# Performance work log

Measured on AMD Instinct MI355X. Metric: run time of the kernel, lower is better.

Reference implementation:

```python
import jax, jax.numpy as jnp
import numpy as np

NEG = -1e30

def setup_inputs() -> dict:
    key = jax.random.key(0)
    k = jax.random.split(key, 6)
    B, Lc, Lq, D = 16, 2048, 256, 256
    c = jax.random.normal(k[0], (B, Lc, D), dtype=jnp.float32)
    q = jax.random.normal(k[1], (B, Lq, D), dtype=jnp.float32)
    c_mask = jnp.ones((B, Lc), dtype=jnp.float32)
    q_mask = jnp.ones((B, Lq), dtype=jnp.float32)
    # xavier-uniform-ish scale for the similarity weights
    lim = float(np.sqrt(6.0 / (D + 1)))
    cq_weight = jax.random.uniform(k[2], (1, 1, D), jnp.float32, -lim, lim)
    c_weight = jax.random.uniform(k[3], (1, D), jnp.float32, -lim, lim)
    q_weight = jax.random.uniform(k[4], (1, D), jnp.float32, -lim, lim)
    bias = jnp.zeros((1,), dtype=jnp.float32)
    return {"c": c, "q": q, "c_mask": c_mask, "q_mask": q_mask,
            "cq_weight": cq_weight, "c_weight": c_weight,
            "q_weight": q_weight, "bias": bias}

def _masked_softmax(logits, mask):
    # mask: 1=keep, 0=pad; broadcast over logits' leading dims
    x = logits * mask + (1.0 - mask) * NEG
    return jax.nn.softmax(x, axis=-1)

def reference(c, q, c_mask, q_mask, cq_weight, c_weight, q_weight, bias):
    # trilinear similarity S[b,i,j] = w_c.c_i + w_q.q_j + (c_i*w_cq).q_j + b
    s0 = jnp.einsum('bid,od->bio', c, c_weight)              # [B,Lc,1]
    s1 = jnp.einsum('bjd,od->boj', q, q_weight)              # [B,1,Lq]
    s2 = jnp.einsum('bid,bjd->bij', c * cq_weight, q)        # [B,Lc,Lq]
    S = s0 + s1 + s2 + bias                                  # [B,Lc,Lq]
    S1 = _masked_softmax(S, q_mask[:, None, :])              # softmax over q
    C2Q = jnp.einsum('bij,bjd->bid', S1, q)                  # [B,Lc,D]
    S2t = _masked_softmax(jnp.swapaxes(S, 1, 2), c_mask[:, None, :])  # [B,Lq,Lc]
    S2 = jnp.einsum('bij,bjk->bik', S1, S2t)                 # [B,Lc,Lc]
    Q2C = jnp.einsum('bik,bkd->bid', S2, c)                  # [B,Lc,D]
    return jnp.concatenate((c, C2Q, c * C2Q, c * Q2C), axis=-1)
```

## Files before the change

### kernel.cpp

```cpp
#include <hip/hip_runtime.h>
#include <hip/hip_bf16.h>

#define NB 16
#define LC 2048
#define LQ 256
#define DD 256
#define NEGINF -1e30f

typedef __attribute__((ext_vector_type(8))) short bf16x8;
typedef __attribute__((ext_vector_type(4))) float f32x4;

#define MFMA16(a, b, c) __builtin_amdgcn_mfma_f32_16x16x32_bf16((a), (b), (c), 0, 0, 0)

typedef const unsigned int __attribute__((address_space(1))) glb_u32;
typedef unsigned int __attribute__((address_space(3))) lds_u32;

__device__ __forceinline__ void gload_lds16(const void* g, void* l) {
    __builtin_amdgcn_global_load_lds((glb_u32*)g, (lds_u32*)l, 16, 0, 0);
}

__device__ __forceinline__ short f2b(float x) {
    unsigned u = __float_as_uint(x);
    unsigned r = (u + 0x7fffu + ((u >> 16) & 1u)) >> 16;
    return (short)r;
}
__device__ __forceinline__ float b2f(short s) {
    return __uint_as_float(((unsigned)(unsigned short)s) << 16);
}

#define NCB (NB * LC / 8)
__global__ __launch_bounds__(256) void prep(
        const float* __restrict__ c, const float* __restrict__ q,
        const float* __restrict__ c_w, const float* __restrict__ cqw,
        const float* __restrict__ q_w, const float* __restrict__ bias,
        short* __restrict__ c16, float* __restrict__ s0c,
        short* __restrict__ qw16, short* __restrict__ qT16,
        float* __restrict__ s1q, float* __restrict__ out) {
    __shared__ float T[64][65];
    int t = threadIdx.x;
    if (blockIdx.x < NCB) {
        int row = blockIdx.x * 8 + (t >> 5);
        int k = t & 31;
        const float* src = c + (size_t)row * DD + k * 8;
        float4 v0 = *(const float4*)(src);
        float4 v1 = *(const float4*)(src + 4);
        float4 w0 = *(const float4*)(c_w + k * 8);
        float4 w1 = *(const float4*)(c_w + k * 8 + 4);
        float s = v0.x * w0.x + v0.y * w0.y + v0.z * w0.z + v0.w * w0.w
                + v1.x * w1.x + v1.y * w1.y + v1.z * w1.z + v1.w * w1.w;
        #pragma unroll
        for (int o = 16; o > 0; o >>= 1) s += __shfl_xor(s, o, 64);
        if (k == 0) s0c[row] = s;
        size_t ob = (size_t)row * (size_t)(4 * DD) + k * 8;
        *(float4*)(out + ob)     = v0;
        *(float4*)(out + ob + 4) = v1;
        ushort4 o0, o1;
        o0.x = (unsigned short)f2b(v0.x); o0.y = (unsigned short)f2b(v0.y);
        o0.z = (unsigned short)f2b(v0.z); o0.w = (unsigned short)f2b(v0.w);
        o1.x = (unsigned short)f2b(v1.x); o1.y = (unsigned short)f2b(v1.y);
        o1.z = (unsigned short)f2b(v1.z); o1.w = (unsigned short)f2b(v1.w);
        ushort4* dst = (ushort4*)(c16 + (size_t)row * DD + k * 8);
        dst[0] = o0;
        dst[1] = o1;
    } else {
        int idx = blockIdx.x - NCB;
        int b = idx >> 2, j0 = (idx & 3) * 64;
        int dd = t & 63, rg = t >> 6;
        float acc[16];
        #pragma unroll
        for (int i = 0; i < 16; ++i) acc[i] = 0.f;
        for (int dc = 0; dc < 4; ++dc) {
            float wv = cqw[dc * 64 + dd];
            float qwv = q_w[dc * 64 + dd];
            #pragma unroll
            for (int rr = 0; rr < 16; ++rr) {
                int r = rg + 4 * rr;
                float v = q[((size_t)b * LQ + j0 + r) * DD + dc * 64 + dd];
                qw16[((size_t)b * LQ + j0 + r) * DD + dc * 64 + dd] = f2b(v * wv);
                acc[rr] += v * qwv;
                T[dd][r] = v;
            }
            __syncthreads();
            int jj = t & 63;
            for (int dw = t >> 6; dw < 64; dw += 4)
                qT16[((size_t)b * DD + dc * 64 + dw) * LQ + j0 + jj] = f2b(T[dw][jj]);
            __syncthreads();
        }
        float bv = bias[0];
        #pragma unroll
        for (int rr = 0; rr < 16; ++rr) {
            float s = acc[rr];
            #pragma unroll
            for (int o = 32; o > 0; o >>= 1) s += __shfl_xor(s, o, 64);
            if (dd == 0) s1q[b * LQ + j0 + rg + 4 * rr] = s + bv;
        }
    }
}

__global__ __launch_bounds__(512) void k1_S(
        const short* __restrict__ c16, const short* __restrict__ qw16,
        const float* __restrict__ cmask, const float* __restrict__ qmask,
        const float* __restrict__ s0c, const float* __restrict__ s1q,
        short* __restrict__ P1b, float* __restrict__ wgtg,
        float* __restrict__ pm, float* __restrict__ ps) {
    __shared__ short As[128 * 64];
    __shared__ short Bs[256 * 64];
    __shared__ float rmLds[128 * 4];
    __shared__ float rsLds[128 * 4];
    __shared__ float rowCLds[128];
    int b  = blockIdx.y;
    int i0 = blockIdx.x * 128;
    int t = threadIdx.x;
    int l = t & 63, w = t >> 6;
    int wr = w >> 2, wc = w & 3;

    f32x4 acc[4][4];
    #pragma unroll
    for (int m = 0; m < 4; ++m)
        #pragma unroll
        for (int n = 0; n < 4; ++n) acc[m][n] = (f32x4){0.f, 0.f, 0.f, 0.f};

    const short* Ag = c16  + ((size_t)b * LC + i0) * DD;
    const short* Bg = qw16 + ((size_t)b * LQ) * DD;
    int lrow = l >> 3;
    int lcolsw = ((l & 7) ^ lrow) * 8;

    for (int kt = 0; kt < DD; kt += 64) {
        __syncthreads();
        #pragma unroll
        for (int r = 0; r < 2; ++r) {
            int chunk = r * 8 + w;
            int row = chunk * 8 + lrow;
            gload_lds16(Ag + (size_t)row * DD + kt + lcolsw, As + chunk * 512);
        }
        #pragma unroll
        for (int r = 0; r < 4; ++r) {
            int chunk = r * 8 + w;
            int row = chunk * 8 + lrow;
            gload_lds16(Bg + (size_t)row * DD + kt + lcolsw, Bs + chunk * 512);
        }
        __syncthreads();
        #pragma unroll
        for (int kf = 0; kf < 2; ++kf) {
            bf16x8 a[4], bb[4];
            #pragma unroll
            for (int m = 0; m < 4; ++m) {
                int row = wr * 64 + m * 16 + (l & 15);
                int byte = row * 128 + kf * 64 + (l >> 4) * 16;
                a[m] = *(const bf16x8*)((const char*)As + (byte ^ ((row & 7) << 4)));
            }
            #pragma unroll
            for (int n = 0; n < 4; ++n) {
                int row = wc * 64 + n * 16 + (l & 15);
                int byte = row * 128 + kf * 64 + (l >> 4) * 16;
                bb[n] = *(const bf16x8*)((const char*)Bs + (byte ^ ((row & 7) << 4)));
            }
            #pragma unroll
            for (int m = 0; m < 4; ++m)
                #pragma unroll
                for (int n = 0; n < 4; ++n)
                    acc[m][n] = MFMA16(a[m], bb[n], acc[m][n]);
        }
    }

    float s1v[4], qmv[4], negq[4];
    #pragma unroll
    for (int n = 0; n < 4; ++n) {
        int j = wc * 64 + n * 16 + (l & 15);
        s1v[n] = s1q[b * LQ + j];
        qmv[n] = qmask[b * LQ + j];
        negq[n] = (1.f - qmv[n]) * NEGINF;
    }
    float s0r[4][4], cmr[4][4];
    #pragma unroll
    for (int m = 0; m < 4; ++m)
        #pragma unroll
        for (int reg = 0; reg < 4; ++reg) {
            int il = wr * 64 + m * 16 + (l >> 4) * 4 + reg;
            s0r[m][reg] = s0c[b * LC + i0 + il];
            cmr[m][reg] = cmask[b * LC + i0 + il];
        }
    #pragma unroll
    for (int m = 0; m < 4; ++m)
        #pragma unroll
        for (int n = 0; n < 4; ++n)
            #pragma unroll
            for (int reg = 0; reg < 4; ++reg)
                acc[m][n][reg] = acc[m][n][reg] + s0r[m][reg] + s1v[n];

    #pragma unroll
    for (int n = 0; n < 4; ++n) {
        float x2v[16];
        float mx = NEGINF;
        #pragma unroll
        for (int m = 0; m < 4; ++m)
            #pragma unroll
            for (int reg = 0; reg < 4; ++reg) {
                float cm = cmr[m][reg];
                float x2 = acc[m][n][reg] * cm + (1.f - cm) * NEGINF;
                x2v[m * 4 + reg] = x2;
                mx = fmaxf(mx, x2);
            }
        float ss = 0.f;
        #pragma unroll
        for (int e = 0; e < 16; ++e) ss += __expf(x2v[e] - mx);
        #pragma unroll
        for (int off = 16; off <= 32; off <<= 1) {
            float om = __shfl_xor(mx, off, 64);
            float os = __shfl_xor(ss, off, 64);
            float nm = fmaxf(mx, om);
            ss = ss * __expf(mx - nm) + os * __expf(om - nm);
            mx = nm;
        }
        if (l < 16) {
            size_t idx = ((size_t)b * 32 + blockIdx.x * 2 + wr) * LQ + wc * 64 + n * 16 + l;
            pm[idx] = mx;
            ps[idx] = ss;
        }
    }

    #pragma unroll
    for (int m = 0; m < 4; ++m)
        #pragma unroll
        for (int reg = 0; reg < 4; ++reg) {
            float mx = NEGINF;
            #pragma unroll
            for (int n = 0; n < 4; ++n)
                mx = fmaxf(mx, fmaf(acc[m][n][reg], qmv[n], negq[n]));
            #pragma unroll
            for (int o = 1; o <= 8; o <<= 1) mx = fmaxf(mx, __shfl_xor(mx, o, 64));
            float ss = 0.f;
            #pragma unroll
            for (int n = 0; n < 4; ++n)
                ss += __expf(fmaf(acc[m][n][reg], qmv[n], negq[n]) - mx);
            #pragma unroll
            for (int o = 1; o <= 8; o <<= 1) ss += __shfl_xor(ss, o, 64);
            if ((l & 15) == 0) {
                int row = wr * 64 + m * 16 + (l >> 4) * 4 + reg;
                rmLds[row * 4 + wc] = mx;
                rsLds[row * 4 + wc] = ss;
            }
        }
    __syncthreads();
    if (t < 128) {
        float m0 = rmLds[t * 4 + 0], m1 = rmLds[t * 4 + 1];
        float m2 = rmLds[t * 4 + 2], m3 = rmLds[t * 4 + 3];
        float mm = fmaxf(fmaxf(m0, m1), fmaxf(m2, m3));
        float ss = rsLds[t * 4 + 0] * __expf(m0 - mm)
                 + rsLds[t * 4 + 1] * __expf(m1 - mm)
                 + rsLds[t * 4 + 2] * __expf(m2 - mm)
                 + rsLds[t * 4 + 3] * __expf(m3 - mm);
        float rc = mm + logf(ss);
        rowCLds[t] = rc;
        wgtg[(size_t)b * LC + i0 + t] = cmask[b * LC + i0 + t] * __expf(rc);
    }
    __syncthreads();

    float rCv[4][4];
    #pragma unroll
    for (int m = 0; m < 4; ++m)
        #pragma unroll
        for (int reg = 0; reg < 4; ++reg)
            rCv[m][reg] = rowCLds[wr * 64 + m * 16 + (l >> 4) * 4 + reg];
    #pragma unroll
    for (int m = 0; m < 4; ++m)
        #pragma unroll
        for (int n = 0; n < 4; ++n)
            #pragma unroll
            for (int reg = 0; reg < 4; ++reg) {
                float p = __expf(fmaf(acc[m][n][reg], qmv[n], negq[n]) - rCv[m][reg]);
                int il = wr * 64 + m * 16 + (l >> 4) * 4 + reg;
                int j = wc * 64 + n * 16 + (l & 15);
                P1b[((size_t)b * LC + i0 + il) * LQ + j] = f2b(p);
            }
}

#define K3S 72
__global__ __launch_bounds__(256) void k3_A2C(
        const short* __restrict__ c16, const short* __restrict__ P1b,
        const float* __restrict__ wgtg,
        const float* __restrict__ pm, const float* __restrict__ ps,
        short* __restrict__ A2CT) {
    __shared__ short As[128 * K3S];
    __shared__ short Bs[128 * K3S];
    __shared__ float colCs[128];
    int b  = blockIdx.y;
    int d0 = (blockIdx.x >> 1) * 128;
    int j0 = (blockIdx.x & 1) * 128;
    int t = threadIdx.x, l = t & 63, w = t >> 6;
    int wr = w >> 1, wc = w & 1;

    if (t < 128) {
        float m = NEGINF, s = 0.f;
        for (int ch = 0; ch < 32; ++ch) {
            float pmv = pm[((size_t)b * 32 + ch) * LQ + j0 + t];
            float psv = ps[((size_t)b * 32 + ch) * LQ + j0 + t];
            float mn = fmaxf(m, pmv);
            s = s * __expf(m - mn) + psv * __expf(pmv - mn);
            m = mn;
        }
        colCs[t] = m + logf(s);
    }

    f32x4 acc[4][4];
    #pragma unroll
    for (int m = 0; m < 4; ++m)
        #pragma unroll
        for (int n = 0; n < 4; ++n) acc[m][n] = (f32x4){0.f, 0.f, 0.f, 0.f};

    int ii4 = (t >> 4) * 4;
    int c8  = (t & 15) * 8;
    int ip  = ii4 ^ (((c8 >> 3) & 7) << 3);
    const size_t gbase = (size_t)b * LC;

    bf16x8 avA[4], pvA[4]; float wvA[4];
    bf16x8 avB[4], pvB[4]; float wvB[4];

    #pragma unroll
    for (int r = 0; r < 4; ++r) {
        size_t gi = gbase + ii4 + r;
        avA[r] = *(const bf16x8*)(c16 + gi * DD + d0 + c8);
        pvA[r] = *(const bf16x8*)(P1b + gi * LQ + j0 + c8);
        wvA[r] = wgtg[gi];
    }

    for (int k0 = 0; k0 < LC; k0 += 128) {
        __syncthreads();
        #pragma unroll
        for (int g = 0; g < 8; ++g) {
            short4 a4, b4;
            a4.x = avA[0][g]; a4.y = avA[1][g]; a4.z = avA[2][g]; a4.w = avA[3][g];
            b4.x = f2b(b2f(pvA[0][g]) * wvA[0]);
            b4.y = f2b(b2f(pvA[1][g]) * wvA[1]);
            b4.z = f2b(b2f(pvA[2][g]) * wvA[2]);
            b4.w = f2b(b2f(pvA[3][g]) * wvA[3]);
            *(short4*)(&As[(c8 + g) * K3S + ip]) = a4;
            *(short4*)(&Bs[(c8 + g) * K3S + ip]) = b4;
        }
        #pragma unroll
        for (int r = 0; r < 4; ++r) {
            size_t gi = gbase + k0 + 64 + ii4 + r;
            avB[r] = *(const bf16x8*)(c16 + gi * DD + d0 + c8);
            pvB[r] = *(const bf16x8*)(P1b + gi * LQ + j0 + c8);
            wvB[r] = wgtg[gi];
        }
        __syncthreads();
        #pragma unroll
        for (int kf = 0; kf < 2; ++kf) {
            bf16x8 a[4], bb[4];
            int colL = kf * 32 + (l >> 4) * 8;
            #pragma unroll
            for (int m = 0; m < 4; ++m) {
                int row = wr * 64 + m * 16 + (l & 15);
                int colP = colL ^ (((row >> 3) & 7) << 3);
                a[m] = *(const bf16x8*)((const char*)As + row * (K3S * 2) + colP * 2);
            }
            #pragma unroll
            for (int n = 0; n < 4; ++n) {
                int row = wc * 64 + n * 16 + (l & 15);
                int colP = colL ^ (((row >> 3) & 7) << 3);
                bb[n] = *(const bf16x8*)((const char*)Bs + row * (K3S * 2) + colP * 2);
            }
            #pragma unroll
            for (int m = 0; m < 4; ++m)
                #pragma unroll
                for (int n = 0; n < 4; ++n)
                    acc[m][n] = MFMA16(a[m], bb[n], acc[m][n]);
        }
        __syncthreads();
        #pragma unroll
        for (int g = 0; g < 8; ++g) {
            short4 a4, b4;
            a4.x = avB[0][g]; a4.y = avB[1][g]; a4.z = avB[2][g]; a4.w = avB[3][g];
            b4.x = f2b(b2f(pvB[0][g]) * wvB[0]);
            b4.y = f2b(b2f(pvB[1][g]) * wvB[1]);
            b4.z = f2b(b2f(pvB[2][g]) * wvB[2]);
            b4.w = f2b(b2f(pvB[3][g]) * wvB[3]);
            *(short4*)(&As[(c8 + g) * K3S + ip]) = a4;
            *(short4*)(&Bs[(c8 + g) * K3S + ip]) = b4;
        }
        if (k0 + 128 < LC) {
            #pragma unroll
            for (int r = 0; r < 4; ++r) {
                size_t gi = gbase + k0 + 128 + ii4 + r;
                avA[r] = *(const bf16x8*)(c16 + gi * DD + d0 + c8);
                pvA[r] = *(const bf16x8*)(P1b + gi * LQ + j0 + c8);
                wvA[r] = wgtg[gi];
            }
        }
        __syncthreads();
        #pragma unroll
        for (int kf = 0; kf < 2; ++kf) {
            bf16x8 a[4], bb[4];
            int colL = kf * 32 + (l >> 4) * 8;
            #pragma unroll
            for (int m = 0; m < 4; ++m) {
                int row = wr * 64 + m * 16 + (l & 15);
                int colP = colL ^ (((row >> 3) & 7) << 3);
                a[m] = *(const bf16x8*)((const char*)As + row * (K3S * 2) + colP * 2);
            }
            #pragma unroll
            for (int n = 0; n < 4; ++n) {
                int row = wc * 64 + n * 16 + (l & 15);
                int colP = colL ^ (((row >> 3) & 7) << 3);
                bb[n] = *(const bf16x8*)((const char*)Bs + row * (K3S * 2) + colP * 2);
            }
            #pragma unroll
            for (int m = 0; m < 4; ++m)
                #pragma unroll
                for (int n = 0; n < 4; ++n)
                    acc[m][n] = MFMA16(a[m], bb[n], acc[m][n]);
        }
    }

    float ec[4];
    #pragma unroll
    for (int n = 0; n < 4; ++n)
        ec[n] = __expf(-colCs[wc * 64 + n * 16 + (l & 15)]);
    #pragma unroll
    for (int m = 0; m < 4; ++m)
        #pragma unroll
        for (int n = 0; n < 4; ++n)
            #pragma unroll
            for (int reg = 0; reg < 4; ++reg) {
                int d = d0 + wr * 64 + m * 16 + (l >> 4) * 4 + reg;
                int j = j0 + wc * 64 + n * 16 + (l & 15);
                A2CT[((size_t)b * DD + d) * LQ + j] = f2b(acc[m][n][reg] * ec[n]);
            }
}

__global__ __launch_bounds__(256) void k4_out(
        const short* __restrict__ P1b, const short* __restrict__ qT16,
        const short* __restrict__ A2CT, const short* __restrict__ c16,
        float* __restrict__ out) {
    __shared__ float Lo1[16][260];
    __shared__ float Lo2[16][260];
    int b = blockIdx.y, i0 = blockIdx.x * 64;
    int t = threadIdx.x, l = t & 63, w = t >> 6;
    int d0w = w * 64;

    f32x4 acc1[4][4], acc2[4][4];
    #pragma unroll
    for (int m = 0; m < 4; ++m)
        #pragma unroll
        for (int n = 0; n < 4; ++n) {
            acc1[m][n] = (f32x4){0.f, 0.f, 0.f, 0.f};
            acc2[m][n] = (f32x4){0.f, 0.f, 0.f, 0.f};
        }
    const short* Sr  = P1b  + ((size_t)b * LC + i0) * LQ;
    const short* qTb = qT16 + (size_t)b * DD * LQ;
    const short* aTb = A2CT + (size_t)b * DD * LQ;

    #pragma unroll 2
    for (int kf = 0; kf < 8; ++kf) {
        int j8 = kf * 32 + (l >> 4) * 8;
        bf16x8 a[4];
        #pragma unroll
        for (int m = 0; m < 4; ++m)
            a[m] = *(const bf16x8*)(Sr + (size_t)(m * 16 + (l & 15)) * LQ + j8);
        #pragma unroll
        for (int n = 0; n < 4; ++n) {
            int d = d0w + n * 16 + (l & 15);
            size_t off = (size_t)d * LQ + j8;
            bf16x8 bq = *(const bf16x8*)(qTb + off);
            bf16x8 ba = *(const bf16x8*)(aTb + off);
            #pragma unroll
            for (int m = 0; m < 4; ++m) {
                acc1[m][n] = MFMA16(a[m], bq, acc1[m][n]);
                acc2[m][n] = MFMA16(a[m], ba, acc2[m][n]);
            }
        }
    }

    const short* cb16 = c16 + (size_t)b * LC * DD;
    #pragma unroll
    for (int m = 0; m < 4; ++m) {
        __syncthreads();
        #pragma unroll
        for (int n = 0; n < 4; ++n) {
            int col = d0w + n * 16 + (l & 15);
            #pragma unroll
            for (int reg = 0; reg < 4; ++reg) {
                int row = (l >> 4) * 4 + reg;
                Lo1[row][col] = acc1[m][n][reg];
                Lo2[row][col] = acc2[m][n][reg];
            }
        }
        __syncthreads();
        #pragma unroll
        for (int rr = 0; rr < 4; ++rr) {
            int row = w * 4 + rr;
            int i = i0 + m * 16 + row;
            float4 f1 = *(const float4*)&Lo1[row][l * 4];
            float4 f2 = *(const float4*)&Lo2[row][l * 4];
            short4 cu = *(const short4*)(cb16 + (size_t)i * DD + l * 4);
            float c0 = b2f(cu.x), c1 = b2f(cu.y), c2 = b2f(cu.z), c3 = b2f(cu.w);
            size_t ob = ((size_t)b * LC + i) * (size_t)(4 * DD);
            float4 p1 = {c0 * f1.x, c1 * f1.y, c2 * f1.z, c3 * f1.w};
            float4 p2 = {c0 * f2.x, c1 * f2.y, c2 * f2.z, c3 * f2.w};
            *(float4*)(out + ob + 256 + l * 4) = f1;
            *(float4*)(out + ob + 512 + l * 4) = p1;
            *(float4*)(out + ob + 768 + l * 4) = p2;
        }
    }
}

extern "C" void kernel_launch(void* const* d_in, const int* in_sizes, int n_in,
                              void* d_out, int out_size, void* d_ws, size_t ws_size,
                              hipStream_t stream) {
    const float* c     = (const float*)d_in[0];
    const float* q     = (const float*)d_in[1];
    const float* cmask = (const float*)d_in[2];
    const float* qmask = (const float*)d_in[3];
    const float* cqw   = (const float*)d_in[4];
    const float* c_w   = (const float*)d_in[5];
    const float* q_w   = (const float*)d_in[6];
    const float* bias  = (const float*)d_in[7];
    float* out = (float*)d_out;

    char* w = (char*)d_ws;
    short* P1b   = (short*)(w);
    short* c16   = (short*)(w + 16777216);
    short* qw16  = (short*)(w + 33554432);
    short* qT16  = (short*)(w + 35651584);
    short* A2CT  = (short*)(w + 37748736);
    float* s0c   = (float*)(w + 39845888);
    float* s1q   = (float*)(w + 39976960);
    float* pm    = (float*)(w + 39993344);
    float* ps    = (float*)(w + 40517632);
    float* wgtg  = (float*)(w + 41041920);

    prep<<<dim3(NCB + NB * LQ / 64), dim3(256), 0, stream>>>(
        c, q, c_w, cqw, q_w, bias, c16, s0c, qw16, qT16, s1q, out);
    k1_S<<<dim3(LC / 128, NB), dim3(512), 0, stream>>>(
        c16, qw16, cmask, qmask, s0c, s1q, P1b, wgtg, pm, ps);
    k3_A2C<<<dim3(4, NB), dim3(256), 0, stream>>>(
        c16, P1b, wgtg, pm, ps, A2CT);
    k4_out<<<dim3(LC / 64, NB), dim3(256), 0, stream>>>(
        P1b, qT16, A2CT, c16, out);
}
```

Baseline: 129.8 us.

## Fuse c conversion into S kernel and split-K the A2C kernel

The c-side preprocessing (bf16 conversion, s0 dot product, copy of c into the output) moves from the prep kernel into k1_S. k1_S now loads fp32 c directly, converts it in registers and stores it to LDS and global, so a separate pass over c is no longer needed. k3_A2C, which previously ran only 64 blocks, is split four ways along the Lc reduction into 256 blocks. The partial sums go to a workspace buffer and an atomic counter lets the last block per tile reduce them and apply the column normalisation. This adds extra partial-sum traffic and makes k1_S's loads of c synchronous instead of async-to-LDS.

```diff
diff --git a/kernel.cpp b/kernel.cpp
--- a/kernel.cpp
+++ b/kernel.cpp
@@ -28,86 +28,60 @@
     return __uint_as_float(((unsigned)(unsigned short)s) << 16);
 }
 
-#define NCB (NB * LC / 8)
-__global__ __launch_bounds__(256) void prep(
-        const float* __restrict__ c, const float* __restrict__ q,
-        const float* __restrict__ c_w, const float* __restrict__ cqw,
+__global__ __launch_bounds__(256) void prep_q(
+        const float* __restrict__ q, const float* __restrict__ cqw,
         const float* __restrict__ q_w, const float* __restrict__ bias,
-        short* __restrict__ c16, float* __restrict__ s0c,
         short* __restrict__ qw16, short* __restrict__ qT16,
-        float* __restrict__ s1q, float* __restrict__ out) {
+        float* __restrict__ s1q, unsigned* __restrict__ cnt) {
     __shared__ float T[64][65];
-    int t = threadIdx.x;
-    if (blockIdx.x < NCB) {
-        int row = blockIdx.x * 8 + (t >> 5);
-        int k = t & 31;
-        const float* src = c + (size_t)row * DD + k * 8;
-        float4 v0 = *(const float4*)(src);
-        float4 v1 = *(const float4*)(src + 4);
-        float4 w0 = *(const float4*)(c_w + k * 8);
-        float4 w1 = *(const float4*)(c_w + k * 8 + 4);
-        float s = v0.x * w0.x + v0.y * w0.y + v0.z * w0.z + v0.w * w0.w
-                + v1.x * w1.x + v1.y * w1.y + v1.z * w1.z + v1.w * w1.w;
-        #pragma unroll
-        for (int o = 16; o > 0; o >>= 1) s += __shfl_xor(s, o, 64);
-        if (k == 0) s0c[row] = s;
-        size_t ob = (size_t)row * (size_t)(4 * DD) + k * 8;
-        *(float4*)(out + ob)     = v0;
-        *(float4*)(out + ob + 4) = v1;
-        ushort4 o0, o1;
-        o0.x = (unsigned short)f2b(v0.x); o0.y = (unsigned short)f2b(v0.y);
-        o0.z = (unsigned short)f2b(v0.z); o0.w = (unsigned short)f2b(v0.w);
-        o1.x = (unsigned short)f2b(v1.x); o1.y = (unsigned short)f2b(v1.y);
-        o1.z = (unsigned short)f2b(v1.z); o1.w = (unsigned short)f2b(v1.w);
-        ushort4* dst = (ushort4*)(c16 + (size_t)row * DD + k * 8);
-        dst[0] = o0;
-        dst[1] = o1;
-    } else {
-        int idx = blockIdx.x - NCB;
-        int b = idx >> 2, j0 = (idx & 3) * 64;
-        int dd = t & 63, rg = t >> 6;
-        float acc[16];
-        #pragma unroll
-        for (int i = 0; i < 16; ++i) acc[i] = 0.f;
-        for (int dc = 0; dc < 4; ++dc) {
-            float wv = cqw[dc * 64 + dd];
-            float qwv = q_w[dc * 64 + dd];
-            #pragma unroll
-            for (int rr = 0; rr < 16; ++rr) {
-                int r = rg + 4 * rr;
-                float v = q[((size_t)b * LQ + j0 + r) * DD + dc * 64 + dd];
-                qw16[((size_t)b * LQ + j0 + r) * DD + dc * 64 + dd] = f2b(v * wv);
-                acc[rr] += v * qwv;
-                T[dd][r] = v;
-            }
-            __syncthreads();
-            int jj = t & 63;
-            for (int dw = t >> 6; dw < 64; dw += 4)
-                qT16[((size_t)b * DD + dc * 64 + dw) * LQ + j0 + jj] = f2b(T[dw][jj]);
-            __syncthreads();
-        }
-        float bv = bias[0];
+    int b = blockIdx.y, j0 = blockIdx.x * 64, t = threadIdx.x;
+    if (blockIdx.x == 0 && blockIdx.y == 0 && t < 64) cnt[t] = 0u;
+    int dd = t & 63, rg = t >> 6;
+    float acc[16];
+    #pragma unroll
+    for (int i = 0; i < 16; ++i) acc[i] = 0.f;
+    for (int dc = 0; dc < 4; ++dc) {
+        float wv = cqw[dc * 64 + dd];
+        float qwv = q_w[dc * 64 + dd];
         #pragma unroll
         for (int rr = 0; rr < 16; ++rr) {
-            float s = acc[rr];
-            #pragma unroll
-            for (int o = 32; o > 0; o >>= 1) s += __shfl_xor(s, o, 64);
-            if (dd == 0) s1q[b * LQ + j0 + rg + 4 * rr] = s + bv;
-        }
+            int r = rg + 4 * rr;
+            float v = q[((size_t)b * LQ + j0 + r) * DD + dc * 64 + dd];
+            qw16[((size_t)b * LQ + j0 + r) * DD + dc * 64 + dd] = f2b(v * wv);
+            acc[rr] += v * qwv;
+            T[dd][r] = v;
+        }
+        __syncthreads();
+        int jj = t & 63;
+        for (int dw = t >> 6; dw < 64; dw += 4)
+            qT16[((size_t)b * DD + dc * 64 + dw) * LQ + j0 + jj] = f2b(T[dw][jj]);
+        __syncthreads();
+    }
+    float bv = bias[0];
+    #pragma unroll
+    for (int rr = 0; rr < 16; ++rr) {
+        float s = acc[rr];
+        #pragma unroll
+        for (int o = 32; o > 0; o >>= 1) s += __shfl_xor(s, o, 64);
+        if (dd == 0) s1q[b * LQ + j0 + rg + 4 * rr] = s + bv;
     }
 }
 
 __global__ __launch_bounds__(512) void k1_S(
-        const short* __restrict__ c16, const short* __restrict__ qw16,
+        const float* __restrict__ c, const short* __restrict__ qw16,
+        const float* __restrict__ c_w,
         const float* __restrict__ cmask, const float* __restrict__ qmask,
-        const float* __restrict__ s0c, const float* __restrict__ s1q,
-        short* __restrict__ P1b, float* __restrict__ wgtg,
-        float* __restrict__ pm, float* __restrict__ ps) {
+        const float* __restrict__ s1q,
+        short* __restrict__ c16, short* __restrict__ P1b,
+        float* __restrict__ wgtg,
+        float* __restrict__ pm, float* __restrict__ ps,
+        float* __restrict__ out) {
     __shared__ short As[128 * 64];
     __shared__ short Bs[256 * 64];
     __shared__ float rmLds[128 * 4];
     __shared__ float rsLds[128 * 4];
     __shared__ float rowCLds[128];
+    __shared__ float s0Lds[128];
     int b  = blockIdx.y;
     int i0 = blockIdx.x * 128;
     int t = threadIdx.x;
@@ -120,25 +94,42 @@
         #pragma unroll
         for (int n = 0; n < 4; ++n) acc[m][n] = (f32x4){0.f, 0.f, 0.f, 0.f};
 
-    const short* Ag = c16  + ((size_t)b * LC + i0) * DD;
+    const float* cg = c + ((size_t)b * LC + i0) * DD;
     const short* Bg = qw16 + ((size_t)b * LQ) * DD;
+    short* c16g = c16 + ((size_t)b * LC + i0) * DD;
     int lrow = l >> 3;
     int lcolsw = ((l & 7) ^ lrow) * 8;
+    int csA = (l & 7) ^ lrow;
+    float s0acc[2] = {0.f, 0.f};
 
     for (int kt = 0; kt < DD; kt += 64) {
         __syncthreads();
-        #pragma unroll
-        for (int r = 0; r < 2; ++r) {
-            int chunk = r * 8 + w;
-            int row = chunk * 8 + lrow;
-            gload_lds16(Ag + (size_t)row * DD + kt + lcolsw, As + chunk * 512);
-        }
         #pragma unroll
         for (int r = 0; r < 4; ++r) {
             int chunk = r * 8 + w;
             int row = chunk * 8 + lrow;
             gload_lds16(Bg + (size_t)row * DD + kt + lcolsw, Bs + chunk * 512);
         }
+        #pragma unroll
+        for (int r = 0; r < 2; ++r) {
+            int chunk = r * 8 + w;
+            int row = chunk * 8 + lrow;
+            const float* src = cg + (size_t)row * DD + kt + csA * 8;
+            float4 v0 = *(const float4*)(src);
+            float4 v1 = *(const float4*)(src + 4);
+            float4 w0 = *(const float4*)(c_w + kt + csA * 8);
+            float4 w1 = *(const float4*)(c_w + kt + csA * 8 + 4);
+            s0acc[r] += v0.x * w0.x + v0.y * w0.y + v0.z * w0.z + v0.w * w0.w
+                      + v1.x * w1.x + v1.y * w1.y + v1.z * w1.z + v1.w * w1.w;
+            bf16x8 pk;
+            pk[0] = f2b(v0.x); pk[1] = f2b(v0.y); pk[2] = f2b(v0.z); pk[3] = f2b(v0.w);
+            pk[4] = f2b(v1.x); pk[5] = f2b(v1.y); pk[6] = f2b(v1.z); pk[7] = f2b(v1.w);
+            *(bf16x8*)(As + chunk * 512 + l * 8) = pk;
+            *(bf16x8*)(c16g + (size_t)row * DD + kt + csA * 8) = pk;
+            size_t ob = ((size_t)b * LC + i0 + row) * (size_t)(4 * DD) + kt + csA * 8;
+            *(float4*)(out + ob)     = v0;
+            *(float4*)(out + ob + 4) = v1;
+        }
         __syncthreads();
         #pragma unroll
         for (int kf = 0; kf < 2; ++kf) {
@@ -162,6 +153,16 @@
                     acc[m][n] = MFMA16(a[m], bb[n], acc[m][n]);
         }
     }
+
+    #pragma unroll
+    for (int r = 0; r < 2; ++r) {
+        float s = s0acc[r];
+        s += __shfl_xor(s, 1, 64);
+        s += __shfl_xor(s, 2, 64);
+        s += __shfl_xor(s, 4, 64);
+        if ((l & 7) == 0) s0Lds[(r * 8 + w) * 8 + lrow] = s;
+    }
+    __syncthreads();
 
     float s1v[4], qmv[4], negq[4];
     #pragma unroll
@@ -177,7 +178,7 @@
         #pragma unroll
         for (int reg = 0; reg < 4; ++reg) {
             int il = wr * 64 + m * 16 + (l >> 4) * 4 + reg;
-            s0r[m][reg] = s0c[b * LC + i0 + il];
+            s0r[m][reg] = s0Lds[il];
             cmr[m][reg] = cmask[b * LC + i0 + il];
         }
     #pragma unroll
@@ -280,27 +281,19 @@
         const short* __restrict__ c16, const short* __restrict__ P1b,
         const float* __restrict__ wgtg,
         const float* __restrict__ pm, const float* __restrict__ ps,
+        float* __restrict__ p3, unsigned* __restrict__ cnt,
         short* __restrict__ A2CT) {
     __shared__ short As[128 * K3S];
     __shared__ short Bs[128 * K3S];
     __shared__ float colCs[128];
-    int b  = blockIdx.y;
-    int d0 = (blockIdx.x >> 1) * 128;
-    int j0 = (blockIdx.x & 1) * 128;
+    __shared__ int lastFlag;
+    int b  = blockIdx.z;
+    int ks = blockIdx.y;
+    int tile = blockIdx.x;
+    int d0 = (tile >> 1) * 128;
+    int j0 = (tile & 1) * 128;
     int t = threadIdx.x, l = t & 63, w = t >> 6;
     int wr = w >> 1, wc = w & 1;
-
-    if (t < 128) {
-        float m = NEGINF, s = 0.f;
-        for (int ch = 0; ch < 32; ++ch) {
-            float pmv = pm[((size_t)b * 32 + ch) * LQ + j0 + t];
-            float psv = ps[((size_t)b * 32 + ch) * LQ + j0 + t];
-            float mn = fmaxf(m, pmv);
-            s = s * __expf(m - mn) + psv * __expf(pmv - mn);
-            m = mn;
-        }
-        colCs[t] = m + logf(s);
-    }
 
     f32x4 acc[4][4];
     #pragma unroll
@@ -311,20 +304,20 @@
     int ii4 = (t >> 4) * 4;
     int c8  = (t & 15) * 8;
     int ip  = ii4 ^ (((c8 >> 3) & 7) << 3);
-    const size_t gbase = (size_t)b * LC;
+    const size_t gb = (size_t)b * LC;
+    const int kend = ks * 512 + 512;
 
     bf16x8 avA[4], pvA[4]; float wvA[4];
     bf16x8 avB[4], pvB[4]; float wvB[4];
-
     #pragma unroll
     for (int r = 0; r < 4; ++r) {
-        size_t gi = gbase + ii4 + r;
+        size_t gi = gb + ks * 512 + ii4 + r;
         avA[r] = *(const bf16x8*)(c16 + gi * DD + d0 + c8);
         pvA[r] = *(const bf16x8*)(P1b + gi * LQ + j0 + c8);
         wvA[r] = wgtg[gi];
     }
 
-    for (int k0 = 0; k0 < LC; k0 += 128) {
+    for (int k0 = ks * 512; k0 < kend; k0 += 128) {
         __syncthreads();
         #pragma unroll
         for (int g = 0; g < 8; ++g) {
@@ -339,7 +332,7 @@
         }
         #pragma unroll
         for (int r = 0; r < 4; ++r) {
-            size_t gi = gbase + k0 + 64 + ii4 + r;
+            size_t gi = gb + k0 + 64 + ii4 + r;
             avB[r] = *(const bf16x8*)(c16 + gi * DD + d0 + c8);
             pvB[r] = *(const bf16x8*)(P1b + gi * LQ + j0 + c8);
             wvB[r] = wgtg[gi];
@@ -379,10 +372,10 @@
             *(short4*)(&As[(c8 + g) * K3S + ip]) = a4;
             *(short4*)(&Bs[(c8 + g) * K3S + ip]) = b4;
         }
-        if (k0 + 128 < LC) {
+        if (k0 + 128 < kend) {
             #pragma unroll
             for (int r = 0; r < 4; ++r) {
-                size_t gi = gbase + k0 + 128 + ii4 + r;
+                size_t gi = gb + k0 + 128 + ii4 + r;
                 avA[r] = *(const bf16x8*)(c16 + gi * DD + d0 + c8);
                 pvA[r] = *(const bf16x8*)(P1b + gi * LQ + j0 + c8);
                 wvA[r] = wgtg[gi];
@@ -413,20 +406,57 @@
         }
     }
 
-    float ec[4];
-    #pragma unroll
-    for (int n = 0; n < 4; ++n)
-        ec[n] = __expf(-colCs[wc * 64 + n * 16 + (l & 15)]);
+    float* P = p3 + (((size_t)b * 4 + ks) * 4 + tile) * 16384;
     #pragma unroll
     for (int m = 0; m < 4; ++m)
         #pragma unroll
         for (int n = 0; n < 4; ++n)
             #pragma unroll
             for (int reg = 0; reg < 4; ++reg) {
-                int d = d0 + wr * 64 + m * 16 + (l >> 4) * 4 + reg;
-                int j = j0 + wc * 64 + n * 16 + (l & 15);
-                A2CT[((size_t)b * DD + d) * LQ + j] = f2b(acc[m][n][reg] * ec[n]);
-            }
+                int ld = wr * 64 + m * 16 + (l >> 4) * 4 + reg;
+                int lj = wc * 64 + n * 16 + (l & 15);
+                P[ld * 128 + lj] = acc[m][n][reg];
+            }
+
+    __syncthreads();
+    if (t == 0) {
+        unsigned old = __hip_atomic_fetch_add(&cnt[b * 4 + tile], 1u,
+                __ATOMIC_ACQ_REL, __HIP_MEMORY_SCOPE_AGENT);
+        lastFlag = (old == 3u);
+    }
+    __syncthreads();
+    if (!lastFlag) return;
+
+    if (t < 128) {
+        float m = NEGINF, s = 0.f;
+        for (int ch = 0; ch < 32; ++ch) {
+            float pmv = pm[((size_t)b * 32 + ch) * LQ + j0 + t];
+            float psv = ps[((size_t)b * 32 + ch) * LQ + j0 + t];
+            float mn = fmaxf(m, pmv);
+            s = s * __expf(m - mn) + psv * __expf(pmv - mn);
+            m = mn;
+        }
+        colCs[t] = m + logf(s);
+    }
+    __syncthreads();
+    const float* pb = p3 + ((size_t)b * 4) * 4 * 16384 + (size_t)tile * 16384;
+    for (int s4 = t; s4 < 4096; s4 += 256) {
+        int ld = s4 >> 5;
+        int lj4 = (s4 & 31) * 4;
+        float4 sum = {0.f, 0.f, 0.f, 0.f};
+        #pragma unroll
+        for (int k2 = 0; k2 < 4; ++k2) {
+            float4 v = *(const float4*)(pb + (size_t)k2 * 4 * 16384 + ld * 128 + lj4);
+            sum.x += v.x; sum.y += v.y; sum.z += v.z; sum.w += v.w;
+        }
+        sum.x *= __expf(-colCs[lj4 + 0]);
+        sum.y *= __expf(-colCs[lj4 + 1]);
+        sum.z *= __expf(-colCs[lj4 + 2]);
+        sum.w *= __expf(-colCs[lj4 + 3]);
+        short4 o;
+        o.x = f2b(sum.x); o.y = f2b(sum.y); o.z = f2b(sum.z); o.w = f2b(sum.w);
+        *(short4*)(A2CT + ((size_t)b * DD + d0 + ld) * LQ + j0 + lj4) = o;
+    }
 }
 
 __global__ __launch_bounds__(256) void k4_out(
@@ -524,18 +554,19 @@
     short* qw16  = (short*)(w + 33554432);
     short* qT16  = (short*)(w + 35651584);
     short* A2CT  = (short*)(w + 37748736);
-    float* s0c   = (float*)(w + 39845888);
     float* s1q   = (float*)(w + 39976960);
     float* pm    = (float*)(w + 39993344);
     float* ps    = (float*)(w + 40517632);
     float* wgtg  = (float*)(w + 41041920);
-
-    prep<<<dim3(NCB + NB * LQ / 64), dim3(256), 0, stream>>>(
-        c, q, c_w, cqw, q_w, bias, c16, s0c, qw16, qT16, s1q, out);
+    float* p3    = (float*)(w + 41172992);
+    unsigned* cnt= (unsigned*)(w + 57950208);
+
+    prep_q<<<dim3(LQ / 64, NB), dim3(256), 0, stream>>>(
+        q, cqw, q_w, bias, qw16, qT16, s1q, cnt);
     k1_S<<<dim3(LC / 128, NB), dim3(512), 0, stream>>>(
-        c16, qw16, cmask, qmask, s0c, s1q, P1b, wgtg, pm, ps);
-    k3_A2C<<<dim3(4, NB), dim3(256), 0, stream>>>(
-        c16, P1b, wgtg, pm, ps, A2CT);
+        c, qw16, c_w, cmask, qmask, s1q, c16, P1b, wgtg, pm, ps, out);
+    k3_A2C<<<dim3(4, 4, NB), dim3(256), 0, stream>>>(
+        c16, P1b, wgtg, pm, ps, p3, cnt, A2CT);
     k4_out<<<dim3(LC / 64, NB), dim3(256), 0, stream>>>(
         P1b, qT16, A2CT, c16, out);
 }
```

Result: faster. 121.4 us (-6.5%).
